# Kernel tuning notes

Measured on AMD Instinct MI355X. Metric: run time of the kernel, lower is better.

## Reference

```python
import jax, jax.numpy as jnp
import numpy as np

K = 64        # top-k from init_kwargs
TAU = 1.0     # temperature at step=0: tau_start*(1-0) + tau_end*0


def setup_inputs() -> dict:
    key = jax.random.key(0)
    k1, k2 = jax.random.split(key)
    B, N = 2048, 8192
    logits = jax.random.normal(k1, (B, N), dtype=jnp.float32)
    # gumbels = -log(Exp(1)) == standard Gumbel noise
    gumbel_noise = jax.random.gumbel(k2, (B, N), dtype=jnp.float32)
    return {"logits": logits, "gumbel_noise": gumbel_noise}


def reference(logits, gumbel_noise):
    # training path of GumbelTopK (step=0 -> tau=TAU, hard=True)
    g = (logits + gumbel_noise) / TAU                       # [B, N]
    order = jnp.argsort(-g, axis=-1)                        # descending sort order
    sorted_g = jnp.take_along_axis(g, order, axis=-1)
    cumsum = jnp.cumsum(jax.nn.softmax(sorted_g, axis=-1), axis=-1)
    mask = (cumsum <= K).astype(sorted_g.dtype)             # NB: faithful to source (<= k)
    sorted_y = mask * jax.nn.softmax(sorted_g / TAU, axis=-1)
    # scatter back to original positions == gather by inverse permutation
    inv = jnp.argsort(order, axis=-1)
    y = jnp.take_along_axis(sorted_y, inv, axis=-1)         # [B, N]
    # hard straight-through: one-hot-k of y
    k = min(K, y.shape[-1])
    _, idx = jax.lax.top_k(y, k)                            # [B, k]
    rows = jnp.arange(y.shape[0])[:, None]
    y_hard = jnp.zeros_like(y).at[rows, idx].set(1.0)
    return jax.lax.stop_gradient(y_hard - y) + y
```

## Files before the change

### kernel.cpp

```cpp
#include <hip/hip_runtime.h>

constexpr int N = 8192;
constexpr int K = 64;
constexpr int THREADS = 256;
constexpr int WAVES = THREADS / 64;
constexpr int EPT = N / THREADS;
constexpr int VEC = EPT / 4;
constexpr int CAP = 1024;

__device__ __forceinline__ unsigned orderable(float f) {
    unsigned x = __float_as_uint(f);
    return (x & 0x80000000u) ? ~x : (x | 0x80000000u);
}

__global__ __launch_bounds__(THREADS, 8)
void gumbel_topk_onehot(const float* __restrict__ logits,
                        const float* __restrict__ noise,
                        float* __restrict__ out)
{
    __shared__ unsigned hist[2048];
    __shared__ unsigned cand[CAP];
    __shared__ unsigned wavesum[WAVES];
    __shared__ unsigned ccount;
    __shared__ unsigned sel_bin, sel_kth, sel_cnt;

    const int tid  = threadIdx.x;
    const int lane = tid & 63;
    const int wave = tid >> 6;
    const long long row = blockIdx.x;

    const float4* lrow = (const float4*)(logits + row * (long long)N);
    const float4* nrow = (const float4*)(noise  + row * (long long)N);

    unsigned key[EPT];
#pragma unroll
    for (int i = 0; i < VEC; ++i) {
        int idx = tid + i * THREADS;
        float4 a = lrow[idx];
        float4 b = nrow[idx];
        key[4*i+0] = orderable(a.x + b.x);
        key[4*i+1] = orderable(a.y + b.y);
        key[4*i+2] = orderable(a.z + b.z);
        key[4*i+3] = orderable(a.w + b.w);
    }

    {
        uint4 z = make_uint4(0,0,0,0);
        for (int i = tid; i < 512; i += THREADS) ((uint4*)hist)[i] = z;
    }
    if (tid == 0) ccount = 0;
    __syncthreads();
#pragma unroll
    for (int e = 0; e < EPT; ++e)
        atomicAdd(&hist[key[e] >> 21], 1u);
    __syncthreads();

    unsigned kth = K;

#define SELECT_BIN(BPT)                                                      \
    {                                                                        \
        unsigned p = 0;                                                      \
        _Pragma("unroll")                                                    \
        for (int j = 0; j < (BPT); ++j) p += hist[tid * (BPT) + j];          \
        unsigned s = p;                                                      \
        _Pragma("unroll")                                                    \
        for (int off = 1; off < 64; off <<= 1) {                             \
            unsigned v = __shfl_down(s, off);                                \
            if (lane + off < 64) s += v;                                     \
        }                                                                    \
        if (lane == 0) wavesum[wave] = s;                                    \
        __syncthreads();                                                     \
        unsigned S = s;                                                      \
        _Pragma("unroll")                                                    \
        for (int w = 0; w < WAVES; ++w) if (w > wave) S += wavesum[w];       \
        unsigned Snext = S - p;                                              \
        if (S >= kth && Snext < kth) {                                       \
            unsigned cum = Snext;                                            \
            for (int j = (BPT) - 1; j >= 0; --j) {                           \
                unsigned c = hist[tid * (BPT) + j];                          \
                if (cum + c >= kth) {                                        \
                    sel_bin = (unsigned)(tid * (BPT) + j);                   \
                    sel_kth = kth - cum;                                     \
                    sel_cnt = c;                                             \
                    break;                                                   \
                }                                                            \
                cum += c;                                                    \
            }                                                                \
        }                                                                    \
        __syncthreads();                                                     \
    }

    SELECT_BIN(8)
    const unsigned b1   = sel_bin;
    const unsigned cnt1 = sel_cnt;
    kth = sel_kth;
    __syncthreads();

    const bool use_cand = (cnt1 <= (unsigned)CAP);
#pragma unroll
    for (int e = 0; e < EPT; ++e) {
        if ((key[e] >> 21) == b1) {
            unsigned pos = atomicAdd(&ccount, 1u);
            if (pos < (unsigned)CAP) cand[pos] = key[e] & 0x1FFFFFu;
        }
    }

    __syncthreads();
    {
        uint4 z = make_uint4(0,0,0,0);
        for (int i = tid; i < 512; i += THREADS) ((uint4*)hist)[i] = z;
    }
    __syncthreads();
    if (use_cand) {
        for (int i = tid; i < (int)cnt1; i += THREADS)
            atomicAdd(&hist[cand[i] >> 10], 1u);
    } else {
#pragma unroll
        for (int e = 0; e < EPT; ++e)
            if ((key[e] >> 21) == b1)
                atomicAdd(&hist[(key[e] >> 10) & 0x7FFu], 1u);
    }
    __syncthreads();

    SELECT_BIN(8)
    const unsigned b2 = sel_bin;
    kth = sel_kth;
    __syncthreads();

    {
        uint4 z = make_uint4(0,0,0,0);
        for (int i = tid; i < 256; i += THREADS) ((uint4*)hist)[i] = z;
    }
    __syncthreads();
    if (use_cand) {
        for (int i = tid; i < (int)cnt1; i += THREADS) {
            unsigned cv = cand[i];
            if ((cv >> 10) == b2) atomicAdd(&hist[cv & 0x3FFu], 1u);
        }
    } else {
        const unsigned pfx = (b1 << 11) | b2;
#pragma unroll
        for (int e = 0; e < EPT; ++e)
            if ((key[e] >> 10) == pfx)
                atomicAdd(&hist[key[e] & 0x3FFu], 1u);
    }
    __syncthreads();

    SELECT_BIN(4)
    const unsigned b3      = sel_bin;
    const unsigned take_eq = sel_kth;
    const unsigned c_eq    = sel_cnt;

    const unsigned T = (b1 << 21) | (b2 << 10) | b3;
    const bool fast = (take_eq == c_eq);

    float4* orow = (float4*)(out + row * (long long)N);
#pragma unroll
    for (int i = 0; i < VEC; ++i) {
        int idx = tid + i * THREADS;
        float4 o;
        o.x = (key[4*i+0] > T || (fast && key[4*i+0] == T)) ? 1.0f : 0.0f;
        o.y = (key[4*i+1] > T || (fast && key[4*i+1] == T)) ? 1.0f : 0.0f;
        o.z = (key[4*i+2] > T || (fast && key[4*i+2] == T)) ? 1.0f : 0.0f;
        o.w = (key[4*i+3] > T || (fast && key[4*i+3] == T)) ? 1.0f : 0.0f;
        orow[idx] = o;
    }

    if (!fast) {
        __syncthreads();
        if (tid == 0) {
            const float* lf = logits + row * (long long)N;
            const float* nf = noise  + row * (long long)N;
            float* of = out + row * (long long)N;
            unsigned c = 0;
            for (int i = 0; i < N; ++i) {
                if (orderable(lf[i] + nf[i]) == T) {
                    of[i] = 1.0f;
                    if (++c == take_eq) break;
                }
            }
        }
    }
#undef SELECT_BIN
}

extern "C" void kernel_launch(void* const* d_in, const int* in_sizes, int n_in,
                              void* d_out, int out_size, void* d_ws, size_t ws_size,
                              hipStream_t stream) {
    const float* logits = (const float*)d_in[0];
    const float* noise  = (const float*)d_in[1];
    float* out = (float*)d_out;
    const int rows = in_sizes[0] / N;
    gumbel_topk_onehot<<<rows, THREADS, 0, stream>>>(logits, noise, out);
}
```

Before: 186.1 us.

## Recompute keys from global memory instead of holding 32 keys in registers

New measurement: 199.3 us. +7.1%, slower.

```diff
diff --git a/kernel.cpp b/kernel.cpp
--- a/kernel.cpp
+++ b/kernel.cpp
@@ -4,8 +4,7 @@
 constexpr int K = 64;
 constexpr int THREADS = 256;
 constexpr int WAVES = THREADS / 64;
-constexpr int EPT = N / THREADS;
-constexpr int VEC = EPT / 4;
+constexpr int VEC = N / THREADS / 4;
 constexpr int CAP = 1024;
 
 __device__ __forceinline__ unsigned orderable(float f) {
@@ -32,27 +31,22 @@
     const float4* lrow = (const float4*)(logits + row * (long long)N);
     const float4* nrow = (const float4*)(noise  + row * (long long)N);
 
-    unsigned key[EPT];
+    {
+        uint4 z = make_uint4(0,0,0,0);
+        for (int i = tid; i < 512; i += THREADS) ((uint4*)hist)[i] = z;
+    }
+    if (tid == 0) ccount = 0;
+    __syncthreads();
 #pragma unroll
     for (int i = 0; i < VEC; ++i) {
         int idx = tid + i * THREADS;
         float4 a = lrow[idx];
         float4 b = nrow[idx];
-        key[4*i+0] = orderable(a.x + b.x);
-        key[4*i+1] = orderable(a.y + b.y);
-        key[4*i+2] = orderable(a.z + b.z);
-        key[4*i+3] = orderable(a.w + b.w);
-    }
-
-    {
-        uint4 z = make_uint4(0,0,0,0);
-        for (int i = tid; i < 512; i += THREADS) ((uint4*)hist)[i] = z;
-    }
-    if (tid == 0) ccount = 0;
-    __syncthreads();
-#pragma unroll
-    for (int e = 0; e < EPT; ++e)
-        atomicAdd(&hist[key[e] >> 21], 1u);
+        atomicAdd(&hist[orderable(a.x + b.x) >> 21], 1u);
+        atomicAdd(&hist[orderable(a.y + b.y) >> 21], 1u);
+        atomicAdd(&hist[orderable(a.z + b.z) >> 21], 1u);
+        atomicAdd(&hist[orderable(a.w + b.w) >> 21], 1u);
+    }
     __syncthreads();
 
     unsigned kth = K;
@@ -97,11 +91,20 @@
     __syncthreads();
 
     const bool use_cand = (cnt1 <= (unsigned)CAP);
-#pragma unroll
-    for (int e = 0; e < EPT; ++e) {
-        if ((key[e] >> 21) == b1) {
-            unsigned pos = atomicAdd(&ccount, 1u);
-            if (pos < (unsigned)CAP) cand[pos] = key[e] & 0x1FFFFFu;
+    if (use_cand) {
+#pragma unroll
+        for (int i = 0; i < VEC; ++i) {
+            int idx = tid + i * THREADS;
+            float4 a = lrow[idx];
+            float4 b = nrow[idx];
+            unsigned k0 = orderable(a.x + b.x);
+            unsigned k1 = orderable(a.y + b.y);
+            unsigned k2 = orderable(a.z + b.z);
+            unsigned k3 = orderable(a.w + b.w);
+            if ((k0 >> 21) == b1) { unsigned p = atomicAdd(&ccount, 1u); if (p < (unsigned)CAP) cand[p] = k0 & 0x1FFFFFu; }
+            if ((k1 >> 21) == b1) { unsigned p = atomicAdd(&ccount, 1u); if (p < (unsigned)CAP) cand[p] = k1 & 0x1FFFFFu; }
+            if ((k2 >> 21) == b1) { unsigned p = atomicAdd(&ccount, 1u); if (p < (unsigned)CAP) cand[p] = k2 & 0x1FFFFFu; }
+            if ((k3 >> 21) == b1) { unsigned p = atomicAdd(&ccount, 1u); if (p < (unsigned)CAP) cand[p] = k3 & 0x1FFFFFu; }
         }
     }
 
@@ -116,9 +119,17 @@
             atomicAdd(&hist[cand[i] >> 10], 1u);
     } else {
 #pragma unroll
-        for (int e = 0; e < EPT; ++e)
-            if ((key[e] >> 21) == b1)
-                atomicAdd(&hist[(key[e] >> 10) & 0x7FFu], 1u);
+        for (int i = 0; i < VEC; ++i) {
+            int idx = tid + i * THREADS;
+            float4 a = lrow[idx];
+            float4 b = nrow[idx];
+            unsigned k0 = orderable(a.x + b.x), k1 = orderable(a.y + b.y);
+            unsigned k2 = orderable(a.z + b.z), k3 = orderable(a.w + b.w);
+            if ((k0 >> 21) == b1) atomicAdd(&hist[(k0 >> 10) & 0x7FFu], 1u);
+            if ((k1 >> 21) == b1) atomicAdd(&hist[(k1 >> 10) & 0x7FFu], 1u);
+            if ((k2 >> 21) == b1) atomicAdd(&hist[(k2 >> 10) & 0x7FFu], 1u);
+            if ((k3 >> 21) == b1) atomicAdd(&hist[(k3 >> 10) & 0x7FFu], 1u);
+        }
     }
     __syncthreads();
 
@@ -140,9 +151,17 @@
     } else {
         const unsigned pfx = (b1 << 11) | b2;
 #pragma unroll
-        for (int e = 0; e < EPT; ++e)
-            if ((key[e] >> 10) == pfx)
-                atomicAdd(&hist[key[e] & 0x3FFu], 1u);
+        for (int i = 0; i < VEC; ++i) {
+            int idx = tid + i * THREADS;
+            float4 a = lrow[idx];
+            float4 b = nrow[idx];
+            unsigned k0 = orderable(a.x + b.x), k1 = orderable(a.y + b.y);
+            unsigned k2 = orderable(a.z + b.z), k3 = orderable(a.w + b.w);
+            if ((k0 >> 10) == pfx) atomicAdd(&hist[k0 & 0x3FFu], 1u);
+            if ((k1 >> 10) == pfx) atomicAdd(&hist[k1 & 0x3FFu], 1u);
+            if ((k2 >> 10) == pfx) atomicAdd(&hist[k2 & 0x3FFu], 1u);
+            if ((k3 >> 10) == pfx) atomicAdd(&hist[k3 & 0x3FFu], 1u);
+        }
     }
     __syncthreads();
 
@@ -158,11 +177,15 @@
 #pragma unroll
     for (int i = 0; i < VEC; ++i) {
         int idx = tid + i * THREADS;
+        float4 a = lrow[idx];
+        float4 b = nrow[idx];
+        unsigned k0 = orderable(a.x + b.x), k1 = orderable(a.y + b.y);
+        unsigned k2 = orderable(a.z + b.z), k3 = orderable(a.w + b.w);
         float4 o;
-        o.x = (key[4*i+0] > T || (fast && key[4*i+0] == T)) ? 1.0f : 0.0f;
-        o.y = (key[4*i+1] > T || (fast && key[4*i+1] == T)) ? 1.0f : 0.0f;
-        o.z = (key[4*i+2] > T || (fast && key[4*i+2] == T)) ? 1.0f : 0.0f;
-        o.w = (key[4*i+3] > T || (fast && key[4*i+3] == T)) ? 1.0f : 0.0f;
+        o.x = (k0 > T || (fast && k0 == T)) ? 1.0f : 0.0f;
+        o.y = (k1 > T || (fast && k1 == T)) ? 1.0f : 0.0f;
+        o.z = (k2 > T || (fast && k2 == T)) ? 1.0f : 0.0f;
+        o.w = (k3 > T || (fast && k3 == T)) ? 1.0f : 0.0f;
         orow[idx] = o;
     }
 
```
